# Kernel tuning notes

Hardware: AMD Instinct MI355X
Metric: run time of the kernel (lower is better)

## Reference

```python
import jax, jax.numpy as jnp
import numpy as np

EPS = 1e-5
AVG_D = 32.0


def setup_inputs() -> dict:
    key = jax.random.key(0)
    ks = jax.random.split(key, 12)
    Ns, Nd, E, D, K = 1_000_000, 100_000, 3_200_000, 16, 2
    Fs, Fd, V = 4, 4, 100_000
    F = Fd + K  # predictor fields
    inp = {}
    inp["Cat_src"] = jax.random.randint(ks[0], (Ns, Fs), 0, V)
    inp["Cat_dst"] = jax.random.randint(ks[1], (Nd, Fd), 0, V)
    inp["src_ids"] = jax.random.randint(ks[2], (E,), 0, Ns)
    inp["dst_ids"] = jax.random.randint(ks[3], (E,), 0, Nd)
    inp["label"] = jax.random.randint(ks[4], (Nd,), 0, 2)
    inp["w"] = jax.random.normal(ks[5], (V, D), dtype=jnp.float32) * 0.05
    inp["W_agg"] = jax.random.normal(ks[6], (K, 12 * D, D), dtype=jnp.float32) * 0.05
    inp["b_agg"] = jnp.zeros((K, D), jnp.float32)
    inp["w_lin"] = jax.random.normal(ks[7], (F * D,), dtype=jnp.float32) * 0.05
    inp["b_lin"] = jnp.zeros((1,), jnp.float32)
    inp["W1"] = jax.random.normal(ks[8], (F * D, 64), dtype=jnp.float32) * 0.05
    inp["b1"] = jnp.zeros((64,), jnp.float32)
    inp["W2"] = jax.random.normal(ks[9], (64, 32), dtype=jnp.float32) * 0.05
    inp["b2"] = jnp.zeros((32,), jnp.float32)
    inp["W3"] = jax.random.normal(ks[10], (32, 1), dtype=jnp.float32) * 0.05
    inp["b3"] = jnp.zeros((1,), jnp.float32)
    return inp


def reference(Cat_src, Cat_dst, src_ids, dst_ids, label, w, W_agg, b_agg,
              w_lin, b_lin, W1, b1, W2, b2, W3, b3):
    Nd = Cat_dst.shape[0]
    # --- node embedding: gather cat fields, RowEmb with modes [mean, max] -> [Ns, K, D]
    emb = w[Cat_src]                                      # [Ns, Fs, D]
    h_src = jnp.stack([emb.mean(1), emb.max(1)], axis=1)  # [Ns, K, D]
    # --- multi-aggregator message passing (copy_u + segment min/max/mean, std via mean of h^2)
    m = h_src[src_ids]                                    # [E, K, D]
    deg = jax.ops.segment_sum(jnp.ones(src_ids.shape, m.dtype), dst_ids, Nd)
    safe = jnp.maximum(deg, 1.0)[:, None, None]
    mean = jax.ops.segment_sum(m, dst_ids, Nd) / safe
    mean2 = jax.ops.segment_sum(m * m, dst_ids, Nd) / safe
    has = (deg > 0)[:, None, None]
    mn = jnp.where(has, jax.ops.segment_min(m, dst_ids, Nd), 0.0)
    mx = jnp.where(has, jax.ops.segment_max(m, dst_ids, Nd), 0.0)
    std = jnp.sqrt(jax.nn.relu(mean2 - mean * mean) + EPS)
    tmp = jnp.concatenate([mean, mn, mx, std], axis=-1)   # [Nd, K, 4D]
    # --- PNA degree scalers: identity / amplification / attenuation
    logd = jnp.log(deg + 1.0)
    log_avg = jnp.log(AVG_D + 1.0)
    amp = (logd / log_avg)[:, None, None]
    att = jnp.where(logd > 0, log_avg / jnp.maximum(logd, EPS), 0.0)[:, None, None]
    scaled = jnp.concatenate([tmp, tmp * amp, tmp * att], axis=-1)  # [Nd, K, 12D]
    mes = jnp.einsum('nkf,kfd->nkd', scaled, W_agg) + b_agg          # [Nd, K, D]
    # --- final block: concat dst cat embeddings with aggregated messages
    x = jnp.concatenate([w[Cat_dst], mes], axis=1)        # [Nd, F, D]
    # --- DeepFM predictor: linear + FM pairwise + deep MLP
    flat = x.reshape(Nd, -1)
    lin = flat @ w_lin + b_lin[0]
    s = x.sum(1)
    fm = 0.5 * ((s * s) - (x * x).sum(1)).sum(-1)
    h = jax.nn.relu(flat @ W1 + b1)
    h = jax.nn.relu(h @ W2 + b2)
    deep = (h @ W3 + b3)[:, 0]
    pred = jax.nn.sigmoid(lin + fm + deep)
    return (pred, label)
```

## Files before the change

kernel.cpp:

```cpp
#include <hip/hip_runtime.h>
#include <math.h>

#define EPSF 1e-5f
#define BSH  5
#define BSZ  32
#define MAXB 4096
#define BCAP 1472
#define XPAD 100
#define X2PADS 72
#define HISTB 512

typedef __attribute__((ext_vector_type(8))) short short8;
typedef __attribute__((ext_vector_type(4))) float float4v;

__device__ inline unsigned f2bf_rne(float x) {
    unsigned u = __float_as_uint(x);
    u += 0x7FFF + ((u >> 16) & 1);
    return u >> 16;
}
__device__ inline short bf16_of(float x) { return (short)f2bf_rne(x); }
__device__ inline float bf2f_lo(unsigned hv) { return __uint_as_float(hv << 16); }
__device__ inline float bf2f_hi(unsigned hv) { return __uint_as_float(hv & 0xFFFF0000u); }
__device__ inline float bf2f_s(ushort s) { return __uint_as_float((unsigned)s << 16); }

__global__ void cast_w(const float* __restrict__ w, ushort* __restrict__ wb, int n) {
    int i4 = (blockIdx.x * 256 + threadIdx.x) * 4;
    if (i4 + 3 < n) {
        float4 v = *(const float4*)(w + i4);
        ushort4 o;
        o.x = (ushort)f2bf_rne(v.x); o.y = (ushort)f2bf_rne(v.y);
        o.z = (ushort)f2bf_rne(v.z); o.w = (ushort)f2bf_rne(v.w);
        *(ushort4*)(wb + i4) = o;
    } else {
        for (int j = i4; j < n; ++j) wb[j] = (ushort)f2bf_rne(w[j]);
    }
}

__global__ __launch_bounds__(256) void build_h_hist(
    const int* __restrict__ Cat_src, const float* __restrict__ w,
    unsigned* __restrict__ h, int Ns,
    const int* __restrict__ dst_ids, int* bcount, int E, int nb)
{
    __shared__ int hsh[MAXB];
    if (blockIdx.x < HISTB) {
        for (int i = threadIdx.x; i < nb; i += 256) hsh[i] = 0;
        __syncthreads();
        int stride = HISTB * 256;
        for (int e = blockIdx.x * 256 + threadIdx.x; e < E; e += stride)
            atomicAdd(&hsh[dst_ids[e] >> BSH], 1);
        __syncthreads();
        for (int i = threadIdx.x; i < nb; i += 256) {
            int c = hsh[i];
            if (c) atomicAdd(&bcount[i], c);
        }
        return;
    }
    int gid = (blockIdx.x - HISTB) * 256 + threadIdx.x;
    int s = gid >> 4;
    if (s >= Ns) return;
    int lane = threadIdx.x & 63;
    int d = lane & 15;
    int c = Cat_src[s * 4 + (d & 3)];
    float vs = 0.f, vm = -INFINITY;
#pragma unroll
    for (int f = 0; f < 4; ++f) {
        int id = __shfl(c, (lane & 48) + f, 64);
        float a = w[id * 16 + d];
        vs += a; vm = fmaxf(vm, a);
    }
    unsigned packed = f2bf_rne(vs * 0.25f) | (f2bf_rne(vm) << 16);
    __builtin_nontemporal_store(packed, &h[s * 16 + d]);
}

__global__ void zero_bcount(int* bcount, int nb) {
    int i = blockIdx.x * 256 + threadIdx.x;
    if (i < nb) bcount[i] = 0;
}

__global__ __launch_bounds__(256) void scan_buckets(const int* __restrict__ bcount,
                                                    int* bstart, int* bcursor, int nb) {
    __shared__ int lsum[256];
    int tid = threadIdx.x;
    int v[16];
    int s = 0;
#pragma unroll
    for (int j = 0; j < 16; ++j) {
        int idx = tid * 16 + j;
        v[j] = (idx < nb) ? bcount[idx] : 0;
        s += v[j];
    }
    lsum[tid] = s;
    __syncthreads();
    for (int off = 1; off < 256; off <<= 1) {
        int y = (tid >= off) ? lsum[tid - off] : 0;
        __syncthreads();
        lsum[tid] += y;
        __syncthreads();
    }
    int run = lsum[tid] - s;
#pragma unroll
    for (int j = 0; j < 16; ++j) {
        int idx = tid * 16 + j;
        if (idx < nb) { bstart[idx] = run; bcursor[idx] = run; }
        run += v[j];
    }
}

__global__ __launch_bounds__(256) void scatter_pairs(
    const int* __restrict__ src_ids, const int* __restrict__ dst_ids,
    int* bcursor, unsigned* __restrict__ pairs, int E, int nb)
{
    __shared__ int cnt[MAXB];
    __shared__ int base[MAXB];
    int tid = threadIdx.x;
    int t0 = blockIdx.x * 8192;
    for (int i = tid; i < nb; i += 256) cnt[i] = 0;
    __syncthreads();
    int rank[32];
#pragma unroll
    for (int j = 0; j < 32; ++j) {
        int e = t0 + j * 256 + tid;
        rank[j] = (e < E) ? atomicAdd(&cnt[dst_ids[e] >> BSH], 1) : 0;
    }
    __syncthreads();
    for (int i = tid; i < nb; i += 256) {
        int c = cnt[i];
        base[i] = c ? atomicAdd(&bcursor[i], c) : 0;
    }
    __syncthreads();
#pragma unroll
    for (int j = 0; j < 32; ++j) {
        int e = t0 + j * 256 + tid;
        if (e < E) {
            int d = dst_ids[e];
            int b = d >> BSH;
            pairs[base[b] + rank[j]] =
                ((unsigned)src_ids[e] << 7) | (unsigned)(d & (BSZ - 1));
        }
    }
}


__device__ inline void bucket_sort(const unsigned* __restrict__ pairs,
                                   int gbase, int cnt,
                                   unsigned* sp, int* hist, int* ofs, int* start,
                                   int tid)
{
    if (tid < BSZ) hist[tid] = 0;
    __syncthreads();
    for (int i = tid; i < cnt; i += 256)
        atomicAdd(&hist[__builtin_nontemporal_load(&pairs[gbase + i]) & (BSZ - 1)], 1);
    __syncthreads();
    if (tid < BSZ) ofs[tid] = hist[tid];
    __syncthreads();
    for (int off = 1; off < BSZ; off <<= 1) {
        int y = (tid < BSZ && tid >= off) ? ofs[tid - off] : 0;
        __syncthreads();
        if (tid < BSZ) ofs[tid] += y;
        __syncthreads();
    }
    if (tid < BSZ) {
        start[tid] = ofs[tid] - hist[tid];
        ofs[tid] = ofs[tid] - hist[tid];
    }
    __syncthreads();
    for (int i = tid; i < cnt; i += 256) {
        unsigned p = __builtin_nontemporal_load(&pairs[gbase + i]);
        int r = atomicAdd(&ofs[p & (BSZ - 1)], 1);
        sp[r] = p;
    }
    __syncthreads();
}

__device__ inline void emit_stats(float sum0, float sq0, float mn0, float mx0,
                                  float sum1, float sq1, float mn1, float mx1,
                                  int dg, int n, int lane, int sub,
                                  ushort* __restrict__ tmpb, int* __restrict__ deg_out)
{
#pragma unroll
    for (int off = 16; off <= 32; off <<= 1) {
        sum0 += __shfl_xor(sum0, off); sq0 += __shfl_xor(sq0, off);
        mn0 = fminf(mn0, __shfl_xor(mn0, off)); mx0 = fmaxf(mx0, __shfl_xor(mx0, off));
        sum1 += __shfl_xor(sum1, off); sq1 += __shfl_xor(sq1, off);
        mn1 = fminf(mn1, __shfl_xor(mn1, off)); mx1 = fmaxf(mx1, __shfl_xor(mx1, off));
    }
    float safe = fmaxf((float)dg, 1.f);
    float r = 1.f / safe;
    bool has = dg > 0;
    float mean0 = sum0 * r, mean1 = sum1 * r;
    float sd0 = sqrtf(fmaxf(sq0 * r - mean0 * mean0, 0.f) + EPSF);
    float sd1 = sqrtf(fmaxf(sq1 * r - mean1 * mean1, 0.f) + EPSF);
    float v0 = (sub == 0) ? mean0 : (sub == 1) ? (has ? mn0 : 0.f)
             : (sub == 2) ? (has ? mx0 : 0.f) : sd0;
    float v1 = (sub == 0) ? mean1 : (sub == 1) ? (has ? mn1 : 0.f)
             : (sub == 2) ? (has ? mx1 : 0.f) : sd1;
    ushort* tp = tmpb + (size_t)n * 128;
    tp[lane] = (ushort)f2bf_rne(v0);
    tp[64 + lane] = (ushort)f2bf_rne(v1);
    if (lane == 0) deg_out[n] = dg;
}

__global__ __launch_bounds__(256) void agg_from_h(
    const unsigned* __restrict__ h,
    const int* __restrict__ bstart, const int* __restrict__ bcount,
    const unsigned* __restrict__ pairs,
    ushort* __restrict__ tmpb, int* __restrict__ deg_out, int Nd)
{
    __shared__ unsigned sp[BCAP];
    __shared__ int hist[BSZ];
    __shared__ int ofs[BSZ];
    __shared__ int start[BSZ];
    int b = blockIdx.x, tid = threadIdx.x;
    int cnt = bcount[b];
    int gbase = bstart[b];
    if (cnt > BCAP) cnt = BCAP;
    bucket_sort(pairs, gbase, cnt, sp, hist, ofs, start, tid);

    int wv = tid >> 6, lane = tid & 63, sub = lane >> 4, d = lane & 15;
#pragma unroll 1
    for (int q = 0; q < 8; ++q) {
        int dl = wv * 8 + q;
        int n = b * BSZ + dl;
        if (n >= Nd) break;
        int st = start[dl], dg = hist[dl];
        float sum0 = 0.f, sq0 = 0.f, mn0 = INFINITY, mx0 = -INFINITY;
        float sum1 = 0.f, sq1 = 0.f, mn1 = INFINITY, mx1 = -INFINITY;
        int nt = (dg + 15) >> 4;
        for (int t = 0; t < nt; ++t) {
            int base = t * 16 + sub;
            unsigned hv[4];
#pragma unroll
            for (int j = 0; j < 4; ++j) {
                int e = base + j * 4;
                int ec = (e < dg) ? e : (dg - 1);
                unsigned p = sp[st + ec];
                hv[j] = h[(p >> 7) * 16 + d];
            }
#pragma unroll
            for (int j = 0; j < 4; ++j) {
                int e = base + j * 4;
                if (e < dg) {
                    float me = bf2f_lo(hv[j]);
                    float vm = bf2f_hi(hv[j]);
                    sum0 += me; sq0 += me * me;
                    mn0 = fminf(mn0, me); mx0 = fmaxf(mx0, me);
                    sum1 += vm; sq1 += vm * vm;
                    mn1 = fminf(mn1, vm); mx1 = fmaxf(mx1, vm);
                }
            }
        }
        emit_stats(sum0, sq0, mn0, mx0, sum1, sq1, mn1, mx1,
                   dg, n, lane, sub, tmpb, deg_out);
    }
}

__global__ __launch_bounds__(256) void agg_from_w(
    const int* __restrict__ Cat_src, const float* __restrict__ w,
    const ushort* __restrict__ wb, int use_bf,
    const int* __restrict__ bstart, const int* __restrict__ bcount,
    const unsigned* __restrict__ pairs,
    ushort* __restrict__ tmpb, int* __restrict__ deg_out, int Nd)
{
    __shared__ unsigned sp[BCAP];
    __shared__ int hist[BSZ];
    __shared__ int ofs[BSZ];
    __shared__ int start[BSZ];
    int b = blockIdx.x, tid = threadIdx.x;
    int cnt = bcount[b];
    int gbase = bstart[b];
    if (cnt > BCAP) cnt = BCAP;
    bucket_sort(pairs, gbase, cnt, sp, hist, ofs, start, tid);

    int wv = tid >> 6, lane = tid & 63, sub = lane >> 4, d = lane & 15;
#pragma unroll 1
    for (int q = 0; q < 8; ++q) {
        int dl = wv * 8 + q;
        int n = b * BSZ + dl;
        if (n >= Nd) break;
        int st = start[dl], dg = hist[dl];
        float sum0 = 0.f, sq0 = 0.f, mn0 = INFINITY, mx0 = -INFINITY;
        float sum1 = 0.f, sq1 = 0.f, mn1 = INFINITY, mx1 = -INFINITY;
        int nt = (dg + 3) >> 2;
        for (int t = 0; t < nt; ++t) {
            int e4 = t * 4 + sub;
            int ec = (e4 < dg) ? e4 : (dg - 1);
            unsigned p = sp[st + ec];
            int src = (int)(p >> 7);
            int cat = Cat_src[src * 4 + (d & 3)];
            float vs = 0.f, vm = -INFINITY;
            if (use_bf) {
#pragma unroll
                for (int f = 0; f < 4; ++f) {
                    int id = __shfl(cat, sub * 16 + f, 64);
                    float a = bf2f_s(wb[id * 16 + d]);
                    vs += a; vm = fmaxf(vm, a);
                }
            } else {
#pragma unroll
                for (int f = 0; f < 4; ++f) {
                    int id = __shfl(cat, sub * 16 + f, 64);
                    float a = w[id * 16 + d];
                    vs += a; vm = fmaxf(vm, a);
                }
            }
            if (e4 < dg) {
                float me = vs * 0.25f;
                sum0 += me; sq0 += me * me;
                mn0 = fminf(mn0, me); mx0 = fmaxf(mx0, me);
                sum1 += vm; sq1 += vm * vm;
                mn1 = fminf(mn1, vm); mx1 = fmaxf(mx1, vm);
            }
        }
        emit_stats(sum0, sq0, mn0, mx0, sum1, sq1, mn1, mx1,
                   dg, n, lane, sub, tmpb, deg_out);
    }
}

__global__ __launch_bounds__(256) void finalize_mfma(
    const int* __restrict__ Cat_dst, const int* __restrict__ label,
    const float* __restrict__ w,
    const float* __restrict__ W_agg, const float* __restrict__ b_agg,
    const float* __restrict__ w_lin, const float* __restrict__ b_lin,
    const float* __restrict__ W1, const float* __restrict__ b1,
    const float* __restrict__ W2, const float* __restrict__ b2,
    const float* __restrict__ W3, const float* __restrict__ b3,
    const int* __restrict__ deg_arr, const ushort* __restrict__ tmpb,
    float* __restrict__ out, int Nd)
{
    __shared__ __align__(16) float sx[4][16 * XPAD];
    __shared__ __align__(16) ushort sx2[4][16 * X2PADS];
    __shared__ float sdeep[4][16];

    int tid = threadIdx.x;
    int wv = tid >> 6, lane = tid & 63;
    int q = lane >> 4, m = lane & 15;
    int n0 = (blockIdx.x * 4 + wv) * 16;
    int n = n0 + m;
    int nc = (n < Nd) ? n : (Nd - 1);

    float* X = sx[wv];
    ushort* X2 = sx2[wv];

    float fdeg = (float)deg_arr[nc];
    float logd = logf(fdeg + 1.f);
    const float logavg = logf(33.0f);
    float amp = logd / logavg;
    float att = (logd > 0.f) ? (logavg / fmaxf(logd, EPSF)) : 0.f;
    float ampr[4], attr[4];
#pragma unroll
    for (int r = 0; r < 4; ++r) {
        ampr[r] = __shfl(amp, q * 4 + r, 64);
        attr[r] = __shfl(att, q * 4 + r, 64);
    }

    const ushort* tpn = tmpb + (size_t)nc * 128;
#pragma unroll
    for (int kvar = 0; kvar < 2; ++kvar) {
        short8 af0 = *(const short8*)(tpn + kvar * 64 + q * 8);
        short8 af1 = *(const short8*)(tpn + kvar * 64 + 32 + q * 8);
        const float* WB = W_agg + kvar * 3072;
        float4v aI = {0.f,0.f,0.f,0.f}, aA = {0.f,0.f,0.f,0.f}, aT = {0.f,0.f,0.f,0.f};
#pragma unroll
        for (int sb = 0; sb < 3; ++sb) {
            short8 b0, b1v;
            const float* bp0 = WB + (sb * 64 + q * 8) * 16 + m;
            const float* bp1 = WB + (sb * 64 + 32 + q * 8) * 16 + m;
#pragma unroll
            for (int j = 0; j < 8; ++j) {
                b0[j]  = bf16_of(bp0[j * 16]);
                b1v[j] = bf16_of(bp1[j * 16]);
            }
            if (sb == 0) {
                aI = __builtin_amdgcn_mfma_f32_16x16x32_bf16(af0, b0, aI, 0, 0, 0);
                aI = __builtin_amdgcn_mfma_f32_16x16x32_bf16(af1, b1v, aI, 0, 0, 0);
            } else if (sb == 1) {
                aA = __builtin_amdgcn_mfma_f32_16x16x32_bf16(af0, b0, aA, 0, 0, 0);
                aA = __builtin_amdgcn_mfma_f32_16x16x32_bf16(af1, b1v, aA, 0, 0, 0);
            } else {
                aT = __builtin_amdgcn_mfma_f32_16x16x32_bf16(af0, b0, aT, 0, 0, 0);
                aT = __builtin_amdgcn_mfma_f32_16x16x32_bf16(af1, b1v, aT, 0, 0, 0);
            }
        }
        float bias = b_agg[kvar * 16 + m];
#pragma unroll
        for (int r = 0; r < 4; ++r)
            X[(q * 4 + r) * XPAD + 64 + kvar * 16 + m] =
                aI[r] + ampr[r] * aA[r] + attr[r] * aT[r] + bias;
    }

    {
        int nl = lane >> 2, fl = lane & 3;
        int nn = n0 + nl;
        int nnc = (nn < Nd) ? nn : (Nd - 1);
        int cid = Cat_dst[nnc * 4 + fl];
        const float4* R = (const float4*)(w + (size_t)cid * 16);
        float* xp = X + nl * XPAD + fl * 16;
        *(float4*)(xp + 0)  = R[0];
        *(float4*)(xp + 4)  = R[1];
        *(float4*)(xp + 8)  = R[2];
        *(float4*)(xp + 12) = R[3];
    }
    __syncthreads();

    float lin = 0.f, sq = 0.f;
    float sd[16];
#pragma unroll
    for (int u = 0; u < 16; ++u) sd[u] = 0.f;
    {
        const float* xp = X + m * XPAD + q * 16;
        const float* wl = w_lin + q * 16;
#pragma unroll
        for (int u = 0; u < 16; ++u) {
            float v = xp[u];
            lin += v * wl[u]; sq += v * v; sd[u] += v;
        }
    }
    if (q < 2) {
        const float* xp = X + m * XPAD + (4 + q) * 16;
        const float* wl = w_lin + (4 + q) * 16;
#pragma unroll
        for (int u = 0; u < 16; ++u) {
            float v = xp[u];
            lin += v * wl[u]; sq += v * v; sd[u] += v;
        }
    }
#pragma unroll
    for (int off = 16; off <= 32; off <<= 1) {
        lin += __shfl_xor(lin, off);
        sq  += __shfl_xor(sq, off);
#pragma unroll
        for (int u = 0; u < 16; ++u) sd[u] += __shfl_xor(sd[u], off);
    }
    float fm = 0.f;
#pragma unroll
    for (int u = 0; u < 16; ++u) fm += sd[u] * sd[u];
    fm = 0.5f * (fm - sq);

    short8 xa[3];
#pragma unroll
    for (int t = 0; t < 3; ++t) {
        const float* xp = X + m * XPAD + t * 32 + q * 8;
        float4 a0 = *(const float4*)xp;
        float4 a1 = *(const float4*)(xp + 4);
        xa[t][0] = bf16_of(a0.x); xa[t][1] = bf16_of(a0.y);
        xa[t][2] = bf16_of(a0.z); xa[t][3] = bf16_of(a0.w);
        xa[t][4] = bf16_of(a1.x); xa[t][5] = bf16_of(a1.y);
        xa[t][6] = bf16_of(a1.z); xa[t][7] = bf16_of(a1.w);
    }
#pragma unroll
    for (int nt = 0; nt < 4; ++nt) {
        float4v acc = {0.f, 0.f, 0.f, 0.f};
#pragma unroll
        for (int t = 0; t < 3; ++t) {
            const float* bp = W1 + (t * 32 + q * 8) * 64 + nt * 16 + m;
            short8 bf;
#pragma unroll
            for (int j = 0; j < 8; ++j) bf[j] = bf16_of(bp[j * 64]);
            acc = __builtin_amdgcn_mfma_f32_16x16x32_bf16(xa[t], bf, acc, 0, 0, 0);
        }
        float bb = b1[nt * 16 + m];
#pragma unroll
        for (int r = 0; r < 4; ++r)
            X2[(q * 4 + r) * X2PADS + nt * 16 + m] =
                (ushort)f2bf_rne(fmaxf(acc[r] + bb, 0.f));
    }
    __syncthreads();

    short8 ha[2];
#pragma unroll
    for (int t = 0; t < 2; ++t)
        ha[t] = *(const short8*)(X2 + m * X2PADS + t * 32 + q * 8);
    float dp[4] = {0.f, 0.f, 0.f, 0.f};
#pragma unroll
    for (int nt = 0; nt < 2; ++nt) {
        float4v acc = {0.f, 0.f, 0.f, 0.f};
#pragma unroll
        for (int t = 0; t < 2; ++t) {
            const float* bp = W2 + (t * 32 + q * 8) * 32 + nt * 16 + m;
            short8 bf;
#pragma unroll
            for (int j = 0; j < 8; ++j) bf[j] = bf16_of(bp[j * 32]);
            acc = __builtin_amdgcn_mfma_f32_16x16x32_bf16(ha[t], bf, acc, 0, 0, 0);
        }
        float bb = b2[nt * 16 + m];
        float w3 = W3[nt * 16 + m];
#pragma unroll
        for (int r = 0; r < 4; ++r)
            dp[r] += fmaxf(acc[r] + bb, 0.f) * w3;
    }
#pragma unroll
    for (int off = 1; off <= 8; off <<= 1) {
#pragma unroll
        for (int r = 0; r < 4; ++r) dp[r] += __shfl_xor(dp[r], off);
    }
    if (m < 4)
        sdeep[wv][q * 4 + m] = (m == 0) ? dp[0] : (m == 1) ? dp[1]
                             : (m == 2) ? dp[2] : dp[3];
    __syncthreads();
    float deep = sdeep[wv][m];

    if (q == 0 && n < Nd) {
        float z = lin + b_lin[0] + fm + deep + b3[0];
        float pred = 1.f / (1.f + expf(-z));
        out[n] = pred;
        out[Nd + n] = (float)label[n];
    }
}

extern "C" void kernel_launch(void* const* d_in, const int* in_sizes, int n_in,
                              void* d_out, int out_size, void* d_ws, size_t ws_size,
                              hipStream_t stream) {
    const int*   Cat_src = (const int*)d_in[0];
    const int*   Cat_dst = (const int*)d_in[1];
    const int*   src_ids = (const int*)d_in[2];
    const int*   dst_ids = (const int*)d_in[3];
    const int*   label   = (const int*)d_in[4];
    const float* w       = (const float*)d_in[5];
    const float* W_agg   = (const float*)d_in[6];
    const float* b_agg   = (const float*)d_in[7];
    const float* w_lin   = (const float*)d_in[8];
    const float* b_lin   = (const float*)d_in[9];
    const float* W1      = (const float*)d_in[10];
    const float* b1      = (const float*)d_in[11];
    const float* W2      = (const float*)d_in[12];
    const float* b2      = (const float*)d_in[13];
    const float* W3      = (const float*)d_in[14];
    const float* b3      = (const float*)d_in[15];

    int E  = in_sizes[2];
    int Nd = in_sizes[4];
    int Ns = in_sizes[0] / 4;
    int VD = in_sizes[5];
    int nb = (Nd + BSZ - 1) >> BSH;

    int* bcount  = (int*)d_ws;
    int* bstart  = bcount + MAXB;
    int* bcursor = bstart + MAXB;
    int* deg     = bcursor + MAXB;
    unsigned* pairs = (unsigned*)(deg + Nd);
    size_t off_tmp = (((size_t)(MAXB * 3 + Nd + E) * 4) + 255) & ~(size_t)255;
    ushort* tmpb = (ushort*)((char*)d_ws + off_tmp);
    ushort* w_bf16 = tmpb + (size_t)Nd * 128;
    unsigned* h  = (unsigned*)(w_bf16 + VD);

    size_t need_common = off_tmp + (size_t)Nd * 256;
    size_t need_A = need_common + (size_t)VD * 2;
    size_t need_B = need_A + (size_t)Ns * 64;
    int mode = (ws_size >= need_B) ? 2 : (ws_size >= need_A) ? 1 : 0;

    float* out = (float*)d_out;

    hipLaunchKernelGGL(zero_bcount, dim3((nb + 255) / 256), dim3(256), 0, stream,
                       bcount, nb);
    if (mode == 2) {
        int hb = (int)(((size_t)Ns * 16 + 255) / 256);
        hipLaunchKernelGGL(build_h_hist, dim3(HISTB + hb), dim3(256), 0, stream,
                           Cat_src, w, h, Ns, dst_ids, bcount, E, nb);
    } else {
        hipLaunchKernelGGL(build_h_hist, dim3(HISTB), dim3(256), 0, stream,
                           Cat_src, w, h, 0, dst_ids, bcount, E, nb);
    }
    hipLaunchKernelGGL(scan_buckets, dim3(1), dim3(256), 0, stream,
                       bcount, bstart, bcursor, nb);
    hipLaunchKernelGGL(scatter_pairs, dim3((E + 8191) / 8192), dim3(256), 0, stream,
                       src_ids, dst_ids, bcursor, pairs, E, nb);
    if (mode == 2) {
        hipLaunchKernelGGL(agg_from_h, dim3(nb), dim3(256), 0, stream,
                           h, bstart, bcount, pairs, tmpb, deg, Nd);
    } else {
        if (mode == 1)
            hipLaunchKernelGGL(cast_w, dim3((VD / 4 + 255) / 256), dim3(256),
                               0, stream, w, w_bf16, VD);
        hipLaunchKernelGGL(agg_from_w, dim3(nb), dim3(256), 0, stream,
                           Cat_src, w, w_bf16, mode, bstart, bcount, pairs,
                           tmpb, deg, Nd);
    }
    hipLaunchKernelGGL(finalize_mfma, dim3((Nd + 63) / 64), dim3(256), 0, stream,
                       Cat_dst, label, w, W_agg, b_agg, w_lin, b_lin,
                       W1, b1, W2, b2, W3, b3, deg, tmpb, out, Nd);
}
```

Baseline: 341.2 us.

## Split edge bucketing into two-pass radix scatter via super-buckets

Replaces the single-pass scatter of edges into 3125 fine buckets with a two-level radix partition. The first pass scatters into 196 super-buckets of 512 destinations using small shared counters. A second kernel then redistributes each super-bucket into its 16 fine buckets. This shrinks the per-block shared histogram and global atomic cursor traffic and should make writes more coalesced, at the cost of an extra pass over E pairs and another E-sized workspace buffer. The pair encoding shifts the source id by 9 bits instead of 7.

Result: no change. 346.0 us (+1.4%).

```diff
diff --git a/kernel.cpp b/kernel.cpp
--- a/kernel.cpp
+++ b/kernel.cpp
@@ -5,6 +5,9 @@
 #define BSH  5
 #define BSZ  32
 #define MAXB 4096
+#define SBH  9
+#define MAXSB 256
+#define TILE 4096
 #define BCAP 1472
 #define XPAD 100
 #define X2PADS 72
@@ -78,7 +81,7 @@
 }
 
 __global__ __launch_bounds__(256) void scan_buckets(const int* __restrict__ bcount,
-                                                    int* bstart, int* bcursor, int nb) {
+                                                    int* bstart, int* sbcursor, int nb) {
     __shared__ int lsum[256];
     int tid = threadIdx.x;
     int v[16];
@@ -98,45 +101,67 @@
         __syncthreads();
     }
     int run = lsum[tid] - s;
+    if (tid * 16 < nb) sbcursor[tid] = run;
 #pragma unroll
     for (int j = 0; j < 16; ++j) {
         int idx = tid * 16 + j;
-        if (idx < nb) { bstart[idx] = run; bcursor[idx] = run; }
+        if (idx < nb) bstart[idx] = run;
         run += v[j];
     }
 }
 
-__global__ __launch_bounds__(256) void scatter_pairs(
+__global__ __launch_bounds__(256) void scatter_sb(
     const int* __restrict__ src_ids, const int* __restrict__ dst_ids,
-    int* bcursor, unsigned* __restrict__ pairs, int E, int nb)
-{
-    __shared__ int cnt[MAXB];
-    __shared__ int base[MAXB];
+    int* sbcursor, unsigned* __restrict__ pairs1, int E, int nsb)
+{
+    __shared__ int cnt[MAXSB];
+    __shared__ int base[MAXSB];
     int tid = threadIdx.x;
-    int t0 = blockIdx.x * 8192;
-    for (int i = tid; i < nb; i += 256) cnt[i] = 0;
-    __syncthreads();
-    int rank[32];
-#pragma unroll
-    for (int j = 0; j < 32; ++j) {
+    int t0 = blockIdx.x * TILE;
+    for (int i = tid; i < nsb; i += 256) cnt[i] = 0;
+    __syncthreads();
+    int rank[TILE / 256];
+#pragma unroll
+    for (int j = 0; j < TILE / 256; ++j) {
         int e = t0 + j * 256 + tid;
-        rank[j] = (e < E) ? atomicAdd(&cnt[dst_ids[e] >> BSH], 1) : 0;
-    }
-    __syncthreads();
-    for (int i = tid; i < nb; i += 256) {
+        rank[j] = (e < E) ? atomicAdd(&cnt[dst_ids[e] >> SBH], 1) : 0;
+    }
+    __syncthreads();
+    for (int i = tid; i < nsb; i += 256) {
         int c = cnt[i];
-        base[i] = c ? atomicAdd(&bcursor[i], c) : 0;
-    }
-    __syncthreads();
-#pragma unroll
-    for (int j = 0; j < 32; ++j) {
+        base[i] = c ? atomicAdd(&sbcursor[i], c) : 0;
+    }
+    __syncthreads();
+#pragma unroll
+    for (int j = 0; j < TILE / 256; ++j) {
         int e = t0 + j * 256 + tid;
         if (e < E) {
             int d = dst_ids[e];
-            int b = d >> BSH;
-            pairs[base[b] + rank[j]] =
-                ((unsigned)src_ids[e] << 7) | (unsigned)(d & (BSZ - 1));
-        }
+            int sb = d >> SBH;
+            pairs1[base[sb] + rank[j]] =
+                ((unsigned)src_ids[e] << 9) | (unsigned)(d & 511);
+        }
+    }
+}
+
+__global__ __launch_bounds__(256) void scatter_fine(
+    const unsigned* __restrict__ pairs1, const int* __restrict__ bstart,
+    unsigned* __restrict__ pairs2, int nb, int nsb, int E)
+{
+    __shared__ int cur[16];
+    int S = blockIdx.x, tid = threadIdx.x;
+    int sbs = bstart[S << 4];
+    int sbe = (S == nsb - 1) ? E : bstart[(S + 1) << 4];
+    if (tid < 16) {
+        int idx = (S << 4) + tid;
+        cur[tid] = (idx < nb) ? bstart[idx] : 0;
+    }
+    __syncthreads();
+    for (int i = sbs + tid; i < sbe; i += 256) {
+        unsigned p = __builtin_nontemporal_load(&pairs1[i]);
+        int fb = (p >> 5) & 15;
+        int pos = atomicAdd(&cur[fb], 1);
+        pairs2[pos] = p;
     }
 }
 
@@ -234,7 +259,7 @@
                 int e = base + j * 4;
                 int ec = (e < dg) ? e : (dg - 1);
                 unsigned p = sp[st + ec];
-                hv[j] = h[(p >> 7) * 16 + d];
+                hv[j] = h[(p >> 9) * 16 + d];
             }
 #pragma unroll
             for (int j = 0; j < 4; ++j) {
@@ -285,7 +310,7 @@
             int e4 = t * 4 + sub;
             int ec = (e4 < dg) ? e4 : (dg - 1);
             unsigned p = sp[st + ec];
-            int src = (int)(p >> 7);
+            int src = (int)(p >> 9);
             int cat = Cat_src[src * 4 + (d & 3)];
             float vs = 0.f, vm = -INFINITY;
             if (use_bf) {
@@ -531,14 +556,17 @@
     int Nd = in_sizes[4];
     int Ns = in_sizes[0] / 4;
     int VD = in_sizes[5];
-    int nb = (Nd + BSZ - 1) >> BSH;
-
-    int* bcount  = (int*)d_ws;
-    int* bstart  = bcount + MAXB;
-    int* bcursor = bstart + MAXB;
-    int* deg     = bcursor + MAXB;
-    unsigned* pairs = (unsigned*)(deg + Nd);
-    size_t off_tmp = (((size_t)(MAXB * 3 + Nd + E) * 4) + 255) & ~(size_t)255;
+    int nb  = (Nd + BSZ - 1) >> BSH;
+    int nsb = (nb + 15) >> 4;
+
+    int* bcount   = (int*)d_ws;
+    int* bstart   = bcount + MAXB;
+    int* sbcursor = bstart + MAXB;
+    int* deg      = sbcursor + MAXSB;
+    unsigned* pairs1 = (unsigned*)(deg + Nd);
+    unsigned* pairs2 = pairs1 + E;
+    size_t off_tmp = (((size_t)(MAXB * 2 + MAXSB + Nd) + 2 * (size_t)E) * 4 + 255)
+                     & ~(size_t)255;
     ushort* tmpb = (ushort*)((char*)d_ws + off_tmp);
     ushort* w_bf16 = tmpb + (size_t)Nd * 128;
     unsigned* h  = (unsigned*)(w_bf16 + VD);
@@ -561,18 +589,20 @@
                            Cat_src, w, h, 0, dst_ids, bcount, E, nb);
     }
     hipLaunchKernelGGL(scan_buckets, dim3(1), dim3(256), 0, stream,
-                       bcount, bstart, bcursor, nb);
-    hipLaunchKernelGGL(scatter_pairs, dim3((E + 8191) / 8192), dim3(256), 0, stream,
-                       src_ids, dst_ids, bcursor, pairs, E, nb);
+                       bcount, bstart, sbcursor, nb);
+    hipLaunchKernelGGL(scatter_sb, dim3((E + TILE - 1) / TILE), dim3(256), 0, stream,
+                       src_ids, dst_ids, sbcursor, pairs1, E, nsb);
+    hipLaunchKernelGGL(scatter_fine, dim3(nsb), dim3(256), 0, stream,
+                       pairs1, bstart, pairs2, nb, nsb, E);
     if (mode == 2) {
         hipLaunchKernelGGL(agg_from_h, dim3(nb), dim3(256), 0, stream,
-                           h, bstart, bcount, pairs, tmpb, deg, Nd);
+                           h, bstart, bcount, pairs2, tmpb, deg, Nd);
     } else {
         if (mode == 1)
             hipLaunchKernelGGL(cast_w, dim3((VD / 4 + 255) / 256), dim3(256),
                                0, stream, w, w_bf16, VD);
         hipLaunchKernelGGL(agg_from_w, dim3(nb), dim3(256), 0, stream,
-                           Cat_src, w, w_bf16, mode, bstart, bcount, pairs,
+                           Cat_src, w, w_bf16, mode, bstart, bcount, pairs2,
                            tmpb, deg, Nd);
     }
     hipLaunchKernelGGL(finalize_mfma, dim3((Nd + 63) / 64), dim3(256), 0, stream,
```
